# Kernel tuning notes

Hardware: AMD Instinct MI355X
Metric: run time of the kernel (lower is better)

## Reference

```python
import jax, jax.numpy as jnp
import numpy as np

N = 131072          # total nodes
E = 4194304         # edges (avg degree 32)
SUB = 16            # size_subgraph_samples
HID = 256


def _gcn_norm(src, dst, n):
    # add self-loops
    loops = jnp.arange(n, dtype=src.dtype)
    src = jnp.concatenate([src, loops])
    dst = jnp.concatenate([dst, loops])
    deg = jax.ops.segment_sum(jnp.ones_like(dst, dtype=jnp.float32), dst, num_segments=n)
    dinv = jnp.where(deg > 0, jax.lax.rsqrt(deg), 0.0)
    norm = dinv[src] * dinv[dst]  # [E+N]
    return src, dst, norm


def _gcn_conv(x, W, b, src, dst, norm, n):
    h = x @ W                                  # [N, out]
    msg = h[src] * norm[:, None]               # gather + scale
    agg = jax.ops.segment_sum(msg, dst, num_segments=n)
    return agg + b


def setup_inputs() -> dict:
    key = jax.random.key(0)
    ks = jax.random.split(key, 6)
    x = jax.random.normal(ks[0], (N, 128), dtype=jnp.float32)
    edge_index = jax.random.randint(ks[1], (2, E), 0, N, dtype=jnp.int64)
    W1 = jax.random.normal(ks[2], (128, HID), dtype=jnp.float32) * (1.0 / np.sqrt(128))
    b1 = jnp.zeros((HID,), dtype=jnp.float32)
    W2 = jax.random.normal(ks[3], (HID, HID), dtype=jnp.float32) * (1.0 / np.sqrt(HID))
    b2 = jnp.zeros((HID,), dtype=jnp.float32)
    Wout = jax.random.normal(ks[4], (HID * SUB, 1), dtype=jnp.float32) * (1.0 / np.sqrt(HID * SUB))
    bout = jnp.zeros((1,), dtype=jnp.float32)
    return {"x": x, "edge_index": edge_index, "W1": W1, "b1": b1,
            "W2": W2, "b2": b2, "Wout": Wout, "bout": bout}


def reference(x, edge_index, W1, b1, W2, b2, Wout, bout):
    n = x.shape[0]
    src, dst, norm = _gcn_norm(edge_index[0], edge_index[1], n)
    h = jax.nn.relu(_gcn_conv(x, W1, b1, src, dst, norm, n))
    h = jax.nn.relu(_gcn_conv(h, W2, b2, src, dst, norm, n))
    h = h.reshape(n // SUB, SUB * h.shape[1])   # [8192, 4096]
    return h @ Wout + bout                       # [8192, 1]
```

## Files before the change

kernel.cpp:

```cpp
#include <hip/hip_runtime.h>
#include <stdint.h>

#define NN 131072
#define NE 4194304
#define BKT 256
#define BKT_SH 9
#define BCAP 20480

typedef __bf16 bf16x8 __attribute__((ext_vector_type(8)));
typedef float  floatx4 __attribute__((ext_vector_type(4)));
typedef unsigned short u16x8 __attribute__((ext_vector_type(8)));

__device__ __forceinline__ float bf2f(unsigned short u) {
  union { unsigned int i; float f; } v; v.i = ((unsigned int)u) << 16; return v.f;
}
__device__ __forceinline__ unsigned short f2bf(float f) {
  union { float f; unsigned int i; } v; v.f = f;
  unsigned int r = v.i + 0x7fffu + ((v.i >> 16) & 1u);
  return (unsigned short)(r >> 16);
}


__global__ __launch_bounds__(256) void k_bzero(int* __restrict__ bktCnt) {
  bktCnt[threadIdx.x] = 0;
}

__global__ __launch_bounds__(1024) void k_bucket(const int* __restrict__ src,
                                                 const int* __restrict__ dst,
                                                 int* __restrict__ bktCnt,
                                                 unsigned int* __restrict__ bktBuf) {
  __shared__ int hist[BKT];
  __shared__ int base[BKT];
  const int t = threadIdx.x;
  if (t < BKT) hist[t] = 0;
  __syncthreads();
  const int e0 = (blockIdx.x * 1024 + t);
  const int4 s = ((const int4*)src)[e0];
  const int4 d = ((const int4*)dst)[e0];
  const int b0 = ((unsigned)d.x) >> BKT_SH, b1 = ((unsigned)d.y) >> BKT_SH;
  const int b2 = ((unsigned)d.z) >> BKT_SH, b3 = ((unsigned)d.w) >> BKT_SH;
  const int r0 = atomicAdd(&hist[b0], 1);
  const int r1 = atomicAdd(&hist[b1], 1);
  const int r2 = atomicAdd(&hist[b2], 1);
  const int r3 = atomicAdd(&hist[b3], 1);
  __syncthreads();
  if (t < BKT) base[t] = atomicAdd(&bktCnt[t], hist[t]);
  __syncthreads();
  const unsigned p0 = (((unsigned)s.x) << BKT_SH) | (d.x & 511);
  const unsigned p1 = (((unsigned)s.y) << BKT_SH) | (d.y & 511);
  const unsigned p2 = (((unsigned)s.z) << BKT_SH) | (d.z & 511);
  const unsigned p3 = (((unsigned)s.w) << BKT_SH) | (d.w & 511);
  bktBuf[(size_t)b0 * BCAP + base[b0] + r0] = p0;
  bktBuf[(size_t)b1 * BCAP + base[b1] + r1] = p1;
  bktBuf[(size_t)b2 * BCAP + base[b2] + r2] = p2;
  bktBuf[(size_t)b3 * BCAP + base[b3] + r3] = p3;
}

__global__ __launch_bounds__(1024) void k_csr(const int* __restrict__ bktCnt,
                                              const unsigned int* __restrict__ bktBuf,
                                              int* __restrict__ row_ptr,
                                              float* __restrict__ dinv,
                                              int* __restrict__ csr) {
  __shared__ int bsum[BKT];
  __shared__ int hist[512];
  __shared__ int sc[512];
  __shared__ int cur[512];
  const int b = blockIdx.x;
  const int t = threadIdx.x;
  if (t < BKT) bsum[t] = bktCnt[t];
  if (t < 512) hist[t] = 0;
  __syncthreads();
  for (int off = 1; off < BKT; off <<= 1) {
    int v = 0;
    if (t < BKT && t >= off) v = bsum[t - off];
    __syncthreads();
    if (t < BKT) bsum[t] += v;
    __syncthreads();
  }
  const int sz = bktCnt[b];
  const int csrBase = bsum[b] - sz;
  const unsigned int* eb = bktBuf + (size_t)b * BCAP;
  for (int i = t; i < sz; i += 1024) atomicAdd(&hist[eb[i] & 511], 1);
  __syncthreads();
  if (t < 512) sc[t] = hist[t];
  __syncthreads();
  for (int off = 1; off < 512; off <<= 1) {
    int v = 0;
    if (t < 512 && t >= off) v = sc[t - off];
    __syncthreads();
    if (t < 512) sc[t] += v;
    __syncthreads();
  }
  if (t < 512) {
    const int ex = csrBase + sc[t] - hist[t];
    row_ptr[b * 512 + t] = ex;
    cur[t] = ex;
    dinv[b * 512 + t] = rsqrtf((float)(hist[t] + 1));
  }
  if (b == BKT - 1 && t == 0) row_ptr[NN] = NE;
  __syncthreads();
  for (int i = t; i < sz; i += 1024) {
    const unsigned e = eb[i];
    csr[atomicAdd(&cur[e & 511], 1)] = (int)(e >> BKT_SH);
  }
}

__global__ __launch_bounds__(256) void k_cvt(const float* __restrict__ X,
                                             unsigned short* __restrict__ Xb) {
  const int t = blockIdx.x * 256 + threadIdx.x;
  const float4 v = ((const float4*)X)[t];
  ushort4 o;
  o.x = f2bf(v.x); o.y = f2bf(v.y); o.z = f2bf(v.z); o.w = f2bf(v.w);
  ((ushort4*)Xb)[t] = o;
}

__global__ __launch_bounds__(256) void k_swizzle(const float* __restrict__ W,
                                                 unsigned short* __restrict__ Wsw) {
  const int t = blockIdx.x * 256 + threadIdx.x;
  const int k = t >> 8, n = t & 255;
  const int s = ((k >> 5) * 16 + (n >> 4)) * 512 + ((k >> 3) & 3) * 128 + (n & 15) * 8 + (k & 7);
  Wsw[s] = f2bf(W[t]);
}

template <int LPR>
__global__ __launch_bounds__(256) void agg_h(const unsigned short* __restrict__ X,
                                             const int* __restrict__ row_ptr,
                                             const int* __restrict__ csr,
                                             const float* __restrict__ dinv,
                                             unsigned short* __restrict__ Y,
                                             int F, int foff) {
  constexpr int SUB = 64 / LPR;
  const int lane = threadIdx.x & 63;
  const int node = (blockIdx.x * blockDim.x + threadIdx.x) >> 6;
  const int sub = lane / LPR;
  const int fl = lane % LPR;
  const int start = row_ptr[node];
  const int end = row_ptr[node + 1];
  const float di = dinv[node];
  float a[8] = {0.f, 0.f, 0.f, 0.f, 0.f, 0.f, 0.f, 0.f};
  const unsigned short* Xf = X + foff + fl * 8;

  for (int e = start; e < end; e += 64) {
    const int nload = min(end - e, 64);
    int s_l = node;
    float w_l = 0.0f;
    if (lane < nload) {
      s_l = __builtin_nontemporal_load(&csr[e + lane]);
      w_l = dinv[s_l];
    }
    for (int j = 0; j < nload; j += 4 * SUB) {
      const int i0 = j + sub, i1 = j + SUB + sub, i2 = j + 2 * SUB + sub, i3 = j + 3 * SUB + sub;
      const int s0 = __shfl(s_l, i0); const float w0 = __shfl(w_l, i0);
      const int s1 = __shfl(s_l, i1); const float w1 = __shfl(w_l, i1);
      const int s2 = __shfl(s_l, i2); const float w2 = __shfl(w_l, i2);
      const int s3 = __shfl(s_l, i3); const float w3 = __shfl(w_l, i3);
      const u16x8 r0 = *(const u16x8*)(Xf + (size_t)s0 * F);
      const u16x8 r1 = *(const u16x8*)(Xf + (size_t)s1 * F);
      const u16x8 r2 = *(const u16x8*)(Xf + (size_t)s2 * F);
      const u16x8 r3 = *(const u16x8*)(Xf + (size_t)s3 * F);
#pragma unroll
      for (int i = 0; i < 8; ++i) a[i] = fmaf(w0, bf2f(r0[i]), a[i]);
#pragma unroll
      for (int i = 0; i < 8; ++i) a[i] = fmaf(w1, bf2f(r1[i]), a[i]);
#pragma unroll
      for (int i = 0; i < 8; ++i) a[i] = fmaf(w2, bf2f(r2[i]), a[i]);
#pragma unroll
      for (int i = 0; i < 8; ++i) a[i] = fmaf(w3, bf2f(r3[i]), a[i]);
    }
  }
#pragma unroll
  for (int off = LPR; off < 64; off <<= 1)
#pragma unroll
    for (int i = 0; i < 8; ++i) a[i] += __shfl_xor(a[i], off);
  const u16x8 sv = *(const u16x8*)(Xf + (size_t)node * F);
#pragma unroll
  for (int i = 0; i < 8; ++i) a[i] = fmaf(di, bf2f(sv[i]), a[i]);
  if (sub == 0) {
    u16x8 o;
#pragma unroll
    for (int i = 0; i < 8; ++i) o[i] = f2bf(di * a[i]);
    *(u16x8*)(Y + (size_t)node * F + foff + fl * 8) = o;
  }
}

template <int K>
__global__ __launch_bounds__(512) void k_gemm(const unsigned short* __restrict__ A,
                                              const unsigned short* __restrict__ Wsw,
                                              const float* __restrict__ bias,
                                              unsigned short* __restrict__ out) {
  __shared__ unsigned short lW[128 * 256];
  const int tid = threadIdx.x;
  const int wave = tid >> 6;
  const int lane = tid & 63;
  const int q = lane >> 4;
  const int m16 = lane & 15;
  const size_t baseM = (size_t)blockIdx.x * 256;

  floatx4 acc[2][16];
#pragma unroll
  for (int t = 0; t < 2; ++t)
#pragma unroll
    for (int nt = 0; nt < 16; ++nt) acc[t][nt] = (floatx4){0.f, 0.f, 0.f, 0.f};

  const size_t rowA0 = baseM + wave * 32 + m16;
  const size_t rowA1 = rowA0 + 16;

  for (int half = 0; half < K / 128; ++half) {
    __syncthreads();
    const uint4* gsrc = (const uint4*)(Wsw + half * 32768);
    uint4* ldst = (uint4*)lW;
#pragma unroll
    for (int i = 0; i < 8; ++i) ldst[i * 512 + tid] = gsrc[i * 512 + tid];
    __syncthreads();

#pragma unroll
    for (int kc = 0; kc < 4; ++kc) {
      const int koff = half * 128 + kc * 32 + q * 8;
      const bf16x8 av0 = *(const bf16x8*)(A + rowA0 * K + koff);
      const bf16x8 av1 = *(const bf16x8*)(A + rowA1 * K + koff);
#pragma unroll
      for (int nt = 0; nt < 16; ++nt) {
        const bf16x8 bv = *(const bf16x8*)(&lW[(kc * 16 + nt) * 512 + lane * 8]);
        acc[0][nt] = __builtin_amdgcn_mfma_f32_16x16x32_bf16(av0, bv, acc[0][nt], 0, 0, 0);
        acc[1][nt] = __builtin_amdgcn_mfma_f32_16x16x32_bf16(av1, bv, acc[1][nt], 0, 0, 0);
      }
    }
  }
  const int rq = (lane >> 4) * 4;
#pragma unroll
  for (int t = 0; t < 2; ++t) {
#pragma unroll
    for (int nt = 0; nt < 16; ++nt) {
      const int col = nt * 16 + m16;
      const float bv = bias[col];
#pragma unroll
      for (int r = 0; r < 4; ++r) {
        const size_t row = baseM + wave * 32 + t * 16 + rq + r;
        float v = acc[t][nt][r] + bv;
        v = fmaxf(v, 0.0f);
        out[row * 256 + col] = f2bf(v);
      }
    }
  }
}

__global__ __launch_bounds__(256) void k_final(const unsigned short* __restrict__ Z,
                                               const float* __restrict__ Wout,
                                               const float* __restrict__ bout,
                                               float* __restrict__ out) {
  const int lane = threadIdx.x & 63;
  const int g = (blockIdx.x * blockDim.x + threadIdx.x) >> 6;
  const unsigned short* z = Z + (size_t)g * 4096;
  float acc = 0.f;
#pragma unroll
  for (int it = 0; it < 16; ++it) {
    const int idx = (it * 64 + lane) * 4;
    const ushort4 zv = *(const ushort4*)(z + idx);
    const float4 wv = *(const float4*)(Wout + idx);
    acc = fmaf(bf2f(zv.x), wv.x, acc);
    acc = fmaf(bf2f(zv.y), wv.y, acc);
    acc = fmaf(bf2f(zv.z), wv.z, acc);
    acc = fmaf(bf2f(zv.w), wv.w, acc);
  }
#pragma unroll
  for (int off = 32; off > 0; off >>= 1) acc += __shfl_down(acc, off);
  if (lane == 0) out[g] = acc + bout[0];
}

extern "C" void kernel_launch(void* const* d_in, const int* in_sizes, int n_in,
                              void* d_out, int out_size, void* d_ws, size_t ws_size,
                              hipStream_t stream) {
  const float* x    = (const float*)d_in[0];
  const int*   ei   = (const int*)d_in[1];
  const float* W1   = (const float*)d_in[2];
  const float* b1   = (const float*)d_in[3];
  const float* W2   = (const float*)d_in[4];
  const float* b2   = (const float*)d_in[5];
  const float* Wout = (const float*)d_in[6];
  const float* bout = (const float*)d_in[7];
  float* out = (float*)d_out;

  char* ws = (char*)d_ws;
  size_t off = 0;
  auto alloc = [&](size_t bytes) {
    char* p = ws + off;
    off += (bytes + 511) & ~(size_t)511;
    return p;
  };
  int*            row_ptr = (int*)alloc(((size_t)NN + 1) * 4);
  float*          dinv    = (float*)alloc((size_t)NN * 4);
  int*            bktCnt  = (int*)alloc(BKT * 4);
  unsigned int*   bktBuf  = (unsigned int*)alloc((size_t)BKT * BCAP * 4);
  int*            csr     = (int*)alloc((size_t)NE * 4);
  unsigned short* Wsw1    = (unsigned short*)alloc(128 * 256 * 2);
  unsigned short* Wsw2    = (unsigned short*)alloc(256 * 256 * 2);
  unsigned short* xb      = (unsigned short*)alloc((size_t)NN * 128 * 2);
  unsigned short* bufA    = (unsigned short*)alloc((size_t)NN * 256 * 2);
  unsigned short* bufB    = (unsigned short*)alloc((size_t)NN * 256 * 2);
  (void)in_sizes; (void)n_in; (void)out_size; (void)ws_size;

  const int* src = ei;
  const int* dst = ei + NE;

  hipLaunchKernelGGL(k_bzero,  dim3(1), dim3(256), 0, stream, bktCnt);
  hipLaunchKernelGGL(k_bucket, dim3(NE / 4096), dim3(1024), 0, stream, src, dst, bktCnt, bktBuf);
  hipLaunchKernelGGL(k_csr,    dim3(BKT), dim3(1024), 0, stream, bktCnt, bktBuf, row_ptr, dinv, csr);
  hipLaunchKernelGGL(k_cvt,    dim3(NN * 128 / 4 / 256), dim3(256), 0, stream, x, xb);
  hipLaunchKernelGGL(k_swizzle, dim3(128), dim3(256), 0, stream, W1, Wsw1);
  hipLaunchKernelGGL(k_swizzle, dim3(256), dim3(256), 0, stream, W2, Wsw2);

  hipLaunchKernelGGL(agg_h<8>, dim3(NN / 4), dim3(256), 0, stream, xb, row_ptr, csr, dinv, bufA, 128, 0);
  hipLaunchKernelGGL(agg_h<8>, dim3(NN / 4), dim3(256), 0, stream, xb, row_ptr, csr, dinv, bufA, 128, 64);
  hipLaunchKernelGGL(k_gemm<128>, dim3(NN / 256), dim3(512), 0, stream, bufA, Wsw1, b1, bufB);
  hipLaunchKernelGGL(agg_h<16>, dim3(NN / 4), dim3(256), 0, stream, bufB, row_ptr, csr, dinv, bufA, 256, 0);
  hipLaunchKernelGGL(agg_h<16>, dim3(NN / 4), dim3(256), 0, stream, bufB, row_ptr, csr, dinv, bufA, 256, 128);
  hipLaunchKernelGGL(k_gemm<256>, dim3(NN / 256), dim3(512), 0, stream, bufA, Wsw2, b2, bufB);
  hipLaunchKernelGGL(k_final, dim3(8192 / 4), dim3(256), 0, stream, bufB, Wout, bout, out);
}
```

Baseline: 733.7 us.

## Split aggregation into narrow 16-feature slices across many launches

Aggregation now uses 2 lanes per row (16 features) and is launched 8 times for layer 1 and 16 times for layer 2, each pass covering one 16-column slice. Each pass gathers a narrow slice per edge, so the gathered feature working set per pass is smaller and more likely to stay in cache. Output stores become nontemporal. In exchange, the CSR indices and dinv are re-read many more times, only 32 bytes are fetched per gathered row, and launch count rises.

```diff
diff --git a/kernel.cpp b/kernel.cpp
--- a/kernel.cpp
+++ b/kernel.cpp
@@ -123,13 +123,14 @@
 }
 
 template <int LPR>
-__global__ __launch_bounds__(256) void agg_h(const unsigned short* __restrict__ X,
+__global__ __launch_bounds__(256) void agg_s(const unsigned short* __restrict__ X,
                                              const int* __restrict__ row_ptr,
                                              const int* __restrict__ csr,
                                              const float* __restrict__ dinv,
                                              unsigned short* __restrict__ Y,
                                              int F, int foff) {
   constexpr int SUB = 64 / LPR;
+  constexpr int L = (4 * SUB <= 64) ? 4 : 64 / SUB;
   const int lane = threadIdx.x & 63;
   const int node = (blockIdx.x * blockDim.x + threadIdx.x) >> 6;
   const int sub = lane / LPR;
@@ -148,24 +149,16 @@
       s_l = __builtin_nontemporal_load(&csr[e + lane]);
       w_l = dinv[s_l];
     }
-    for (int j = 0; j < nload; j += 4 * SUB) {
-      const int i0 = j + sub, i1 = j + SUB + sub, i2 = j + 2 * SUB + sub, i3 = j + 3 * SUB + sub;
-      const int s0 = __shfl(s_l, i0); const float w0 = __shfl(w_l, i0);
-      const int s1 = __shfl(s_l, i1); const float w1 = __shfl(w_l, i1);
-      const int s2 = __shfl(s_l, i2); const float w2 = __shfl(w_l, i2);
-      const int s3 = __shfl(s_l, i3); const float w3 = __shfl(w_l, i3);
-      const u16x8 r0 = *(const u16x8*)(Xf + (size_t)s0 * F);
-      const u16x8 r1 = *(const u16x8*)(Xf + (size_t)s1 * F);
-      const u16x8 r2 = *(const u16x8*)(Xf + (size_t)s2 * F);
-      const u16x8 r3 = *(const u16x8*)(Xf + (size_t)s3 * F);
-#pragma unroll
-      for (int i = 0; i < 8; ++i) a[i] = fmaf(w0, bf2f(r0[i]), a[i]);
-#pragma unroll
-      for (int i = 0; i < 8; ++i) a[i] = fmaf(w1, bf2f(r1[i]), a[i]);
-#pragma unroll
-      for (int i = 0; i < 8; ++i) a[i] = fmaf(w2, bf2f(r2[i]), a[i]);
-#pragma unroll
-      for (int i = 0; i < 8; ++i) a[i] = fmaf(w3, bf2f(r3[i]), a[i]);
+    for (int j = 0; j < nload; j += L * SUB) {
+#pragma unroll
+      for (int l = 0; l < L; ++l) {
+        const int idx = j + l * SUB + sub;
+        const int s = __shfl(s_l, idx);
+        const float w = __shfl(w_l, idx);
+        const u16x8 r = *(const u16x8*)(Xf + (size_t)s * F);
+#pragma unroll
+        for (int i = 0; i < 8; ++i) a[i] = fmaf(w, bf2f(r[i]), a[i]);
+      }
     }
   }
 #pragma unroll
@@ -179,7 +172,7 @@
     u16x8 o;
 #pragma unroll
     for (int i = 0; i < 8; ++i) o[i] = f2bf(di * a[i]);
-    *(u16x8*)(Y + (size_t)node * F + foff + fl * 8) = o;
+    __builtin_nontemporal_store(o, (u16x8*)(Y + (size_t)node * F + foff + fl * 8));
   }
 }
 
@@ -309,11 +302,13 @@
   hipLaunchKernelGGL(k_swizzle, dim3(128), dim3(256), 0, stream, W1, Wsw1);
   hipLaunchKernelGGL(k_swizzle, dim3(256), dim3(256), 0, stream, W2, Wsw2);
 
-  hipLaunchKernelGGL(agg_h<8>, dim3(NN / 4), dim3(256), 0, stream, xb, row_ptr, csr, dinv, bufA, 128, 0);
-  hipLaunchKernelGGL(agg_h<8>, dim3(NN / 4), dim3(256), 0, stream, xb, row_ptr, csr, dinv, bufA, 128, 64);
+  for (int p = 0; p < 8; ++p)
+    hipLaunchKernelGGL(agg_s<2>, dim3(NN / 4), dim3(256), 0, stream,
+                       xb, row_ptr, csr, dinv, bufA, 128, 16 * p);
   hipLaunchKernelGGL(k_gemm<128>, dim3(NN / 256), dim3(512), 0, stream, bufA, Wsw1, b1, bufB);
-  hipLaunchKernelGGL(agg_h<16>, dim3(NN / 4), dim3(256), 0, stream, bufB, row_ptr, csr, dinv, bufA, 256, 0);
-  hipLaunchKernelGGL(agg_h<16>, dim3(NN / 4), dim3(256), 0, stream, bufB, row_ptr, csr, dinv, bufA, 256, 128);
+  for (int p = 0; p < 16; ++p)
+    hipLaunchKernelGGL(agg_s<2>, dim3(NN / 4), dim3(256), 0, stream,
+                       bufB, row_ptr, csr, dinv, bufA, 256, 16 * p);
   hipLaunchKernelGGL(k_gemm<256>, dim3(NN / 256), dim3(512), 0, stream, bufA, Wsw2, b2, bufB);
   hipLaunchKernelGGL(k_final, dim3(8192 / 4), dim3(256), 0, stream, bufB, Wout, bout, out);
 }
```

Result: slower. 2.000 ms (+172.6%).

## Fuse final linear projection into layer-2 GEMM epilogue and merge layer-1 aggregation passes

Applied to the files above, without the earlier changes.

The layer-2 GEMM epilogue now applies bias and ReLU, dots each output row with the matching slice of Wout, and reduces across the wave to write the final scalar per 16-node group. This removes the bf16 write and re-read of the 131072x256 layer-2 activation and the separate final kernel. The layer-1 aggregation now covers all 128 features in one launch with 16 lanes per row instead of two 64-feature passes, so the CSR and dinv are read once instead of twice for that layer. In exchange, each aggregation lane group processes more neighbours serially, and the epilogue issues extra Wout loads per element.

```diff
diff --git a/kernel.cpp b/kernel.cpp
--- a/kernel.cpp
+++ b/kernel.cpp
@@ -122,18 +122,16 @@
   Wsw[s] = f2bf(W[t]);
 }
 
-template <int LPR>
 __global__ __launch_bounds__(256) void agg_h(const unsigned short* __restrict__ X,
                                              const int* __restrict__ row_ptr,
                                              const int* __restrict__ csr,
                                              const float* __restrict__ dinv,
                                              unsigned short* __restrict__ Y,
                                              int F, int foff) {
-  constexpr int SUB = 64 / LPR;
   const int lane = threadIdx.x & 63;
   const int node = (blockIdx.x * blockDim.x + threadIdx.x) >> 6;
-  const int sub = lane / LPR;
-  const int fl = lane % LPR;
+  const int sub = lane >> 4;
+  const int fl = lane & 15;
   const int start = row_ptr[node];
   const int end = row_ptr[node + 1];
   const float di = dinv[node];
@@ -148,8 +146,8 @@
       s_l = __builtin_nontemporal_load(&csr[e + lane]);
       w_l = dinv[s_l];
     }
-    for (int j = 0; j < nload; j += 4 * SUB) {
-      const int i0 = j + sub, i1 = j + SUB + sub, i2 = j + 2 * SUB + sub, i3 = j + 3 * SUB + sub;
+    for (int j = 0; j < nload; j += 16) {
+      const int i0 = j + sub, i1 = j + 4 + sub, i2 = j + 8 + sub, i3 = j + 12 + sub;
       const int s0 = __shfl(s_l, i0); const float w0 = __shfl(w_l, i0);
       const int s1 = __shfl(s_l, i1); const float w1 = __shfl(w_l, i1);
       const int s2 = __shfl(s_l, i2); const float w2 = __shfl(w_l, i2);
@@ -169,9 +167,9 @@
     }
   }
 #pragma unroll
-  for (int off = LPR; off < 64; off <<= 1)
-#pragma unroll
-    for (int i = 0; i < 8; ++i) a[i] += __shfl_xor(a[i], off);
+  for (int i = 0; i < 8; ++i) a[i] += __shfl_xor(a[i], 16);
+#pragma unroll
+  for (int i = 0; i < 8; ++i) a[i] += __shfl_xor(a[i], 32);
   const u16x8 sv = *(const u16x8*)(Xf + (size_t)node * F);
 #pragma unroll
   for (int i = 0; i < 8; ++i) a[i] = fmaf(di, bf2f(sv[i]), a[i]);
@@ -244,27 +242,77 @@
   }
 }
 
-__global__ __launch_bounds__(256) void k_final(const unsigned short* __restrict__ Z,
-                                               const float* __restrict__ Wout,
-                                               const float* __restrict__ bout,
-                                               float* __restrict__ out) {
-  const int lane = threadIdx.x & 63;
-  const int g = (blockIdx.x * blockDim.x + threadIdx.x) >> 6;
-  const unsigned short* z = Z + (size_t)g * 4096;
-  float acc = 0.f;
-#pragma unroll
-  for (int it = 0; it < 16; ++it) {
-    const int idx = (it * 64 + lane) * 4;
-    const ushort4 zv = *(const ushort4*)(z + idx);
-    const float4 wv = *(const float4*)(Wout + idx);
-    acc = fmaf(bf2f(zv.x), wv.x, acc);
-    acc = fmaf(bf2f(zv.y), wv.y, acc);
-    acc = fmaf(bf2f(zv.z), wv.z, acc);
-    acc = fmaf(bf2f(zv.w), wv.w, acc);
-  }
-#pragma unroll
-  for (int off = 32; off > 0; off >>= 1) acc += __shfl_down(acc, off);
-  if (lane == 0) out[g] = acc + bout[0];
+__global__ __launch_bounds__(512) void k_gemm_out(const unsigned short* __restrict__ A,
+                                                  const unsigned short* __restrict__ Wsw,
+                                                  const float* __restrict__ bias,
+                                                  const float* __restrict__ Wout,
+                                                  const float* __restrict__ bout,
+                                                  float* __restrict__ out) {
+  constexpr int K = 256;
+  __shared__ unsigned short lW[128 * 256];
+  const int tid = threadIdx.x;
+  const int wave = tid >> 6;
+  const int lane = tid & 63;
+  const int q = lane >> 4;
+  const int m16 = lane & 15;
+  const size_t baseM = (size_t)blockIdx.x * 256;
+
+  floatx4 acc[2][16];
+#pragma unroll
+  for (int t = 0; t < 2; ++t)
+#pragma unroll
+    for (int nt = 0; nt < 16; ++nt) acc[t][nt] = (floatx4){0.f, 0.f, 0.f, 0.f};
+
+  const size_t rowA0 = baseM + wave * 32 + m16;
+  const size_t rowA1 = rowA0 + 16;
+
+  for (int half = 0; half < 2; ++half) {
+    __syncthreads();
+    const uint4* gsrc = (const uint4*)(Wsw + half * 32768);
+    uint4* ldst = (uint4*)lW;
+#pragma unroll
+    for (int i = 0; i < 8; ++i) ldst[i * 512 + tid] = gsrc[i * 512 + tid];
+    __syncthreads();
+
+#pragma unroll
+    for (int kc = 0; kc < 4; ++kc) {
+      const int koff = half * 128 + kc * 32 + q * 8;
+      const bf16x8 av0 = *(const bf16x8*)(A + rowA0 * K + koff);
+      const bf16x8 av1 = *(const bf16x8*)(A + rowA1 * K + koff);
+#pragma unroll
+      for (int nt = 0; nt < 16; ++nt) {
+        const bf16x8 bv = *(const bf16x8*)(&lW[(kc * 16 + nt) * 512 + lane * 8]);
+        acc[0][nt] = __builtin_amdgcn_mfma_f32_16x16x32_bf16(av0, bv, acc[0][nt], 0, 0, 0);
+        acc[1][nt] = __builtin_amdgcn_mfma_f32_16x16x32_bf16(av1, bv, acc[1][nt], 0, 0, 0);
+      }
+    }
+  }
+  const int rq = (lane >> 4) * 4;
+  float p0 = 0.f, p1 = 0.f;
+#pragma unroll
+  for (int nt = 0; nt < 16; ++nt) {
+    const int col = nt * 16 + m16;
+    const float bv = bias[col];
+#pragma unroll
+    for (int r = 0; r < 4; ++r) {
+      const float wv = Wout[(rq + r) * 256 + col];
+      const float v0 = fmaxf(acc[0][nt][r] + bv, 0.0f);
+      const float v1 = fmaxf(acc[1][nt][r] + bv, 0.0f);
+      p0 = fmaf(v0, wv, p0);
+      p1 = fmaf(v1, wv, p1);
+    }
+  }
+#pragma unroll
+  for (int off = 32; off > 0; off >>= 1) {
+    p0 += __shfl_xor(p0, off);
+    p1 += __shfl_xor(p1, off);
+  }
+  if (lane == 0) {
+    const float bo = bout[0];
+    const int g = blockIdx.x * 16 + wave * 2;
+    out[g]     = p0 + bo;
+    out[g + 1] = p1 + bo;
+  }
 }
 
 extern "C" void kernel_launch(void* const* d_in, const int* in_sizes, int n_in,
@@ -309,11 +357,9 @@
   hipLaunchKernelGGL(k_swizzle, dim3(128), dim3(256), 0, stream, W1, Wsw1);
   hipLaunchKernelGGL(k_swizzle, dim3(256), dim3(256), 0, stream, W2, Wsw2);
 
-  hipLaunchKernelGGL(agg_h<8>, dim3(NN / 4), dim3(256), 0, stream, xb, row_ptr, csr, dinv, bufA, 128, 0);
-  hipLaunchKernelGGL(agg_h<8>, dim3(NN / 4), dim3(256), 0, stream, xb, row_ptr, csr, dinv, bufA, 128, 64);
+  hipLaunchKernelGGL(agg_h, dim3(NN / 4), dim3(256), 0, stream, xb, row_ptr, csr, dinv, bufA, 128, 0);
   hipLaunchKernelGGL(k_gemm<128>, dim3(NN / 256), dim3(512), 0, stream, bufA, Wsw1, b1, bufB);
-  hipLaunchKernelGGL(agg_h<16>, dim3(NN / 4), dim3(256), 0, stream, bufB, row_ptr, csr, dinv, bufA, 256, 0);
-  hipLaunchKernelGGL(agg_h<16>, dim3(NN / 4), dim3(256), 0, stream, bufB, row_ptr, csr, dinv, bufA, 256, 128);
-  hipLaunchKernelGGL(k_gemm<256>, dim3(NN / 256), dim3(512), 0, stream, bufA, Wsw2, b2, bufB);
-  hipLaunchKernelGGL(k_final, dim3(8192 / 4), dim3(256), 0, stream, bufB, Wout, bout, out);
-}
+  hipLaunchKernelGGL(agg_h, dim3(NN / 4), dim3(256), 0, stream, bufB, row_ptr, csr, dinv, bufA, 256, 0);
+  hipLaunchKernelGGL(agg_h, dim3(NN / 4), dim3(256), 0, stream, bufB, row_ptr, csr, dinv, bufA, 256, 128);
+  hipLaunchKernelGGL(k_gemm_out, dim3(NN / 256), dim3(512), 0, stream, bufA, Wsw2, b2, Wout, bout, out);
+}
```

Result: faster. 710.1 us (-3.2%).
